# Kernel optimization log

Measured on AMD Instinct MI355X. Metric: run time of the kernel, lower is better.

## Reference

```python
import jax, jax.numpy as jnp
import numpy as np
from math import factorial, pi, sqrt

LMAX = 5
MUL_IN = 128
NUM_CHANNELS = 4
NUM_RADII = 20
RES_BETA = 180
RES_ALPHA = 359
IRREPS_DIM = (LMAX + 1) ** 2  # 36
NUM_GRAPHS = 32
NUM_SPECIES = 5


def _sh_grid_matrix():
    """Real spherical harmonics evaluated on a Gauss-Legendre (beta) x uniform (alpha) grid.

    Returns Y of shape [RES_BETA, RES_ALPHA, IRREPS_DIM]; this is the dense form of
    e3nn's to_s2grid (Legendre x Fourier) transform matrix.
    """
    y, _ = np.polynomial.legendre.leggauss(RES_BETA)  # y = cos(beta), quadrature='gausslegendre'
    alpha = 2.0 * np.pi * np.arange(RES_ALPHA) / RES_ALPHA
    # Associated Legendre P_l^m(y) (no Condon-Shortley), shape [l, m, RES_BETA]
    P = np.zeros((LMAX + 1, LMAX + 1, RES_BETA))
    P[0, 0] = 1.0
    sy = np.sqrt(np.maximum(1.0 - y * y, 0.0))
    for m in range(1, LMAX + 1):
        P[m, m] = (2 * m - 1) * sy * P[m - 1, m - 1]
    for m in range(LMAX):
        P[m + 1, m] = (2 * m + 1) * y * P[m, m]
    for m in range(LMAX + 1):
        for l in range(m + 2, LMAX + 1):
            P[l, m] = ((2 * l - 1) * y * P[l - 1, m] - (l + m - 1) * P[l - 2, m]) / (l - m)
    Y = np.zeros((RES_BETA, RES_ALPHA, IRREPS_DIM))
    idx = 0
    for l in range(LMAX + 1):
        for m in range(-l, l + 1):
            am = abs(m)
            K = sqrt((2 * l + 1) / (4.0 * pi) * factorial(l - am) / factorial(l + am))
            if m == 0:
                Y[:, :, idx] = (K * P[l, 0])[:, None]
            elif m > 0:
                Y[:, :, idx] = sqrt(2.0) * K * P[l, m][:, None] * np.cos(m * alpha)[None, :]
            else:
                Y[:, :, idx] = sqrt(2.0) * K * P[l, am][:, None] * np.sin(am * alpha)[None, :]
            idx += 1
    return Y.astype(np.float32)


def setup_inputs() -> dict:
    key = jax.random.key(0)
    k1, k2, k3, k4 = jax.random.split(key, 4)
    focus = jax.random.normal(k1, (NUM_GRAPHS, MUL_IN * IRREPS_DIM), dtype=jnp.float32)
    embed_table = jax.random.normal(k2, (NUM_SPECIES, MUL_IN * (LMAX + 1)), dtype=jnp.float32)
    linear_weights = jax.random.normal(k3, (LMAX + 1, MUL_IN, NUM_RADII * NUM_CHANNELS), dtype=jnp.float32)
    target_species = jax.random.randint(k4, (NUM_GRAPHS,), 0, NUM_SPECIES)
    return {
        "focus_node_embeddings": focus,
        "embed_table": embed_table,
        "linear_weights": linear_weights,
        "target_species": target_species,
    }


def reference(focus_node_embeddings, embed_table, linear_weights, target_species):
    G = focus_node_embeddings.shape[0]
    Y = jnp.asarray(_sh_grid_matrix())  # [B, A, 36]
    emb = embed_table[target_species]  # [G, num_irreps = 768], one scalar per irrep channel
    inv_sqrt_fan = 1.0 / np.sqrt(MUL_IN).astype(np.float32)

    coeffs = []
    off_in, off_emb = 0, 0
    for l in range(LMAX + 1):
        dim_m = 2 * l + 1
        # irreps-block view: [G, mul_in, 2l+1]
        x_l = focus_node_embeddings[:, off_in:off_in + MUL_IN * dim_m].reshape(G, MUL_IN, dim_m)
        # per-irrep scalar gating (target_species_embeddings * focus_node_embeddings)
        x_l = x_l * emb[:, off_emb:off_emb + MUL_IN, None]
        # equivariant Linear: mixes multiplicities only, per m, fan-in normalized
        y_l = jnp.einsum("gim,io->gom", x_l, linear_weights[l]) * inv_sqrt_fan
        # mul_to_axis(num_channels) then mul_to_axis(num_radii)
        coeffs.append(y_l.reshape(G, NUM_CHANNELS, NUM_RADII, dim_m))
        off_in += MUL_IN * dim_m
        off_emb += MUL_IN
    position_coeffs = jnp.concatenate(coeffs, axis=-1)  # [G, C, R, 36]

    # to_s2grid: coefficients -> spherical grid signal
    grid = jnp.einsum("gcri,bai->gcrba", position_coeffs, Y)  # [G, C, R, B, A]
    # logsumexp over channels, then max-normalize per graph
    logits = jax.scipy.special.logsumexp(grid, axis=1)  # [G, R, B, A]
    logits = logits - logits.max(axis=(-3, -2, -1), keepdims=True)
    return position_coeffs, logits
```

## Files before the change

kernel.cpp:

```cpp
#include <hip/hip_runtime.h>

#define G_N    32
#define MUL    128
#define RADII  20
#define CH     4
#define RES_B  180
#define RES_A  359
#define IDIM   36
#define COEFF_N (G_N*CH*RADII*IDIM)
#define NCHUNK 5
#define BCH_BLK 36
#define BCH_W   9

typedef float v2f __attribute__((ext_vector_type(2)));

__device__ __forceinline__ float fexp2(float x){
#if __has_builtin(__builtin_amdgcn_exp2f)
  return __builtin_amdgcn_exp2f(x);
#else
  return exp2f(x);
#endif
}
__device__ __forceinline__ float flog2(float x){
#if __has_builtin(__builtin_amdgcn_logf)
  return __builtin_amdgcn_logf(x);
#else
  return log2f(x);
#endif
}
__device__ __forceinline__ unsigned enc_f(float f){
  unsigned u = __float_as_uint(f);
  return (u & 0x80000000u) ? ~u : (u | 0x80000000u);
}
__device__ __forceinline__ float dec_f(unsigned k){
  return __uint_as_float((k & 0x80000000u) ? (k ^ 0x80000000u) : ~k);
}

__global__ __launch_bounds__(256) void fused_prep_kernel(
                              const float* __restrict__ focus, const float* __restrict__ embt,
                              const float* __restrict__ W, const int* __restrict__ tspec,
                              float* __restrict__ out,
                              float* __restrict__ PYs, float* __restrict__ Ftab){
  __shared__ double ak[RES_B + 1], bk[RES_B + 1];
  int blk = blockIdx.x;
  int t   = threadIdx.x;
  if (blk == 360){
    const double PI = 3.14159265358979323846;
    const double LOG2E = 1.4426950408889634074;
    if (t >= 2 && t <= RES_B){
      ak[t] = (2.0*t - 1.0) / (double)t;
      bk[t] = (t - 1.0) / (double)t;
    }
    __syncthreads();
    if (t < RES_B){
      int i = RES_B - 1 - t;
      double x = cos(PI * (i + 0.75) / (RES_B + 0.5));
      for (int it = 0; it < 3; ++it){
        double p0 = 1.0, p1 = x;
        for (int k = 2; k <= RES_B; ++k){
          double t1 = ak[k] * x;
          double pk = fma(t1, p1, -(bk[k] * p0));
          p0 = p1; p1 = pk;
        }
        x -= p1 * (x*x - 1.0) / ((double)RES_B * (x*p1 - p0));
      }
      double y = x;
      double sy = sqrt(fmax(1.0 - y*y, 0.0));
      double P[6][6];
      P[0][0] = 1.0;
      for (int m = 1; m < 6; ++m) P[m][m] = (2.0*m - 1.0)*sy*P[m-1][m-1];
      for (int m = 0; m < 5; ++m) P[m+1][m] = (2.0*m + 1.0)*y*P[m][m];
      for (int m = 0; m < 6; ++m)
        for (int l = m + 2; l < 6; ++l)
          P[l][m] = ((2.0*l - 1.0)*y*P[l-1][m] - (l + m - 1.0)*P[l-2][m]) / (double)(l - m);
      const double fact[11] = {1,1,2,6,24,120,720,5040,40320,362880,3628800};
      for (int l = 0; l < 6; ++l)
        for (int m = 0; m <= l; ++m){
          double K = sqrt((2.0*l + 1.0)/(4.0*PI)*fact[l-m]/fact[l+m]);
          double v = K * P[l][m] * LOG2E;
          if (m > 0) v *= sqrt(2.0);
          PYs[t*36 + l*6 + m] = (float)v;
        }
    }
    for (int a = t; a < RES_A; a += 256){
      double al = 2.0*PI*a/(double)RES_A;
      Ftab[a*12 + 0] = 1.0f;
      for (int m = 1; m <= 5; ++m){
        Ftab[a*12 + m]     = (float)cos(m*al);
        Ftab[a*12 + 5 + m] = (float)sin(m*al);
      }
      Ftab[a*12 + 11] = 0.f;
    }
  } else {
    int idx = blk * 256 + t;
    int i36 = idx % IDIM;
    int go  = idx / IDIM;
    int o   = go % (CH*RADII);
    int g   = go / (CH*RADII);
    int l   = (int)sqrtf((float)i36 + 0.5f);
    int mo  = i36 - l*l;
    int dim = 2*l + 1;
    const float* fp = focus + g*(MUL*IDIM) + MUL*l*l + mo;
    const float* ep = embt + tspec[g]*(MUL*6) + MUL*l;
    const float* wp = W + l*(MUL*80) + o;
    float s = 0.f;
    #pragma unroll 4
    for (int i = 0; i < MUL; ++i)
      s = fmaf(fp[i*dim] * ep[i], wp[i*80], s);
    out[idx] = s * 0.088388347648318447f;
  }
}

template<int WRITE>
__global__ __launch_bounds__(256, 4) void compute_kernel(const float* __restrict__ coeffs,
                          const float* __restrict__ PYs, const float* __restrict__ Ftab,
                          float* __restrict__ out, unsigned* __restrict__ gmax){
  int blk   = blockIdx.x;
  int chunk = blk % NCHUNK;
  int gr    = blk / NCHUNK;
  int r = gr % RADII;
  int g = gr / RADII;
  int tid  = threadIdx.x;
  int wave = tid >> 6, lane = tid & 63;
  int b0   = chunk * BCH_BLK;

  __shared__ float cv[CH][IDIM];
  __shared__ __align__(16) float tmpa[BCH_BLK][12][4];
  __shared__ float wred[4];

  for (int v = tid; v < CH*IDIM; v += 256){
    int c = v / IDIM, i = v % IDIM;
    cv[c][i] = coeffs[((g*CH + c)*RADII + r)*IDIM + i];
  }
  float nsub = 0.f;
  if (WRITE) nsub = -flog2(dec_f(gmax[g])) * 0.69314718055994531f;
  float f0[11], f1[11], f2[11];
  {
    const float4* Fq = reinterpret_cast<const float4*>(Ftab);
    float4 a0 = Fq[lane*3],       a1 = Fq[lane*3+1],       a2 = Fq[lane*3+2];
    float4 b0v = Fq[(lane+64)*3], b1 = Fq[(lane+64)*3+1],  b2 = Fq[(lane+64)*3+2];
    float4 c0 = Fq[(lane+128)*3], c1 = Fq[(lane+128)*3+1], c2 = Fq[(lane+128)*3+2];
    f0[0]=a0.x; f0[1]=a0.y; f0[2]=a0.z; f0[3]=a0.w; f0[4]=a1.x; f0[5]=a1.y;
    f0[6]=a1.z; f0[7]=a1.w; f0[8]=a2.x; f0[9]=a2.y; f0[10]=a2.z;
    f1[0]=b0v.x; f1[1]=b0v.y; f1[2]=b0v.z; f1[3]=b0v.w; f1[4]=b1.x; f1[5]=b1.y;
    f1[6]=b1.z; f1[7]=b1.w; f1[8]=b2.x; f1[9]=b2.y; f1[10]=b2.z;
    f2[0]=c0.x; f2[1]=c0.y; f2[2]=c0.z; f2[3]=c0.w; f2[4]=c1.x; f2[5]=c1.y;
    f2[6]=c1.z; f2[7]=c1.w; f2[8]=c2.x; f2[9]=c2.y; f2[10]=c2.z;
  }
  __syncthreads();

  for (int v = tid; v < BCH_BLK*44; v += 256){
    int bl = v / 44, cm = v % 44;
    int c = cm / 11, mm = cm % 11;
    int am, ii;
    if (mm == 0)      { am = 0;      ii = 0;        }
    else if (mm <= 5) { am = mm;     ii = mm;       }
    else              { am = mm - 5; ii = -(mm-5);  }
    const float* py = PYs + (b0 + bl)*36 + am;
    float s = 0.f;
    for (int l = am; l < 6; ++l)
      s = fmaf(cv[c][l*l + l + ii], py[l*6], s);
    tmpa[bl][mm][c] = s;
  }
  __syncthreads();

  const float LN2 = 0.69314718055994531f;
  float smx[3] = {0.f, 0.f, 0.f};
  bool tail_ok = (lane < 52);
  float* row = out + ((size_t)gr*RES_B + b0 + wave*BCH_W)*RES_A;
  for (int bl = 0; bl < BCH_W; ++bl){
    const float4* tq = reinterpret_cast<const float4*>(&tmpa[wave*BCH_W + bl][0][0]);
    v2f C01[3], C23[3], S01[3], S23[3];
    {
      float4 qv = tq[0];
      v2f a = {qv.x, qv.y}, b = {qv.z, qv.w};
      #pragma unroll
      for (int k = 0; k < 3; ++k){ C01[k] = a; C23[k] = b; }
    }
    #pragma unroll
    for (int mm = 1; mm <= 5; ++mm){
      float4 qv = tq[mm];
      v2f a = {qv.x, qv.y}, b = {qv.z, qv.w};
      C01[0] = __builtin_elementwise_fma(a, (v2f){f0[mm], f0[mm]}, C01[0]);
      C23[0] = __builtin_elementwise_fma(b, (v2f){f0[mm], f0[mm]}, C23[0]);
      C01[1] = __builtin_elementwise_fma(a, (v2f){f1[mm], f1[mm]}, C01[1]);
      C23[1] = __builtin_elementwise_fma(b, (v2f){f1[mm], f1[mm]}, C23[1]);
      C01[2] = __builtin_elementwise_fma(a, (v2f){f2[mm], f2[mm]}, C01[2]);
      C23[2] = __builtin_elementwise_fma(b, (v2f){f2[mm], f2[mm]}, C23[2]);
    }
    {
      float4 qv = tq[6];
      v2f a = {qv.x, qv.y}, b = {qv.z, qv.w};
      S01[0] = a * (v2f){f0[6], f0[6]};  S23[0] = b * (v2f){f0[6], f0[6]};
      S01[1] = a * (v2f){f1[6], f1[6]};  S23[1] = b * (v2f){f1[6], f1[6]};
      S01[2] = a * (v2f){f2[6], f2[6]};  S23[2] = b * (v2f){f2[6], f2[6]};
    }
    #pragma unroll
    for (int mm = 7; mm <= 10; ++mm){
      float4 qv = tq[mm];
      v2f a = {qv.x, qv.y}, b = {qv.z, qv.w};
      S01[0] = __builtin_elementwise_fma(a, (v2f){f0[mm], f0[mm]}, S01[0]);
      S23[0] = __builtin_elementwise_fma(b, (v2f){f0[mm], f0[mm]}, S23[0]);
      S01[1] = __builtin_elementwise_fma(a, (v2f){f1[mm], f1[mm]}, S01[1]);
      S23[1] = __builtin_elementwise_fma(b, (v2f){f1[mm], f1[mm]}, S23[1]);
      S01[2] = __builtin_elementwise_fma(a, (v2f){f2[mm], f2[mm]}, S01[2]);
      S23[2] = __builtin_elementwise_fma(b, (v2f){f2[mm], f2[mm]}, S23[2]);
    }
    #pragma unroll
    for (int k = 0; k < 3; ++k){
      v2f hp0 = C01[k] + S01[k], hp1 = C23[k] + S23[k];
      v2f hm0 = C01[k] - S01[k], hm1 = C23[k] - S23[k];
      float sp = (fexp2(hp0.x) + fexp2(hp0.y)) + (fexp2(hp1.x) + fexp2(hp1.y));
      float sm = (fexp2(hm0.x) + fexp2(hm0.y)) + (fexp2(hm1.x) + fexp2(hm1.y));
      if (WRITE){
        if (k < 2 || tail_ok){
          int p = lane + 64*k;
          row[p] = fmaf(flog2(sp), LN2, nsub);
          if (p) row[359 - p] = fmaf(flog2(sm), LN2, nsub);
        }
      } else {
        smx[k] = fmaxf(smx[k], fmaxf(sp, sm));
      }
    }
    row += RES_A;
  }
  if (!WRITE){
    float smax = fmaxf(fmaxf(smx[0], smx[1]), smx[2]);
    #pragma unroll
    for (int off = 32; off > 0; off >>= 1)
      smax = fmaxf(smax, __shfl_xor(smax, off, 64));
    if (lane == 0) wred[wave] = smax;
    __syncthreads();
    if (tid == 0){
      float m = fmaxf(fmaxf(wred[0], wred[1]), fmaxf(wred[2], wred[3]));
      atomicMax(gmax + g, enc_f(m));
    }
  }
}

extern "C" void kernel_launch(void* const* d_in, const int* in_sizes, int n_in,
                              void* d_out, int out_size, void* d_ws, size_t ws_size,
                              hipStream_t stream){
  const float* focus = (const float*)d_in[0];
  const float* embt  = (const float*)d_in[1];
  const float* W     = (const float*)d_in[2];
  const int*   tspec = (const int*)d_in[3];
  float* out = (float*)d_out;
  float* ws  = (float*)d_ws;
  unsigned* gmax = (unsigned*)d_ws;
  float* PYs  = ws + 32;
  float* Ftab = ws + 32 + RES_B*36;

  hipMemsetAsync(d_ws, 0, 128, stream);
  fused_prep_kernel<<<361, 256, 0, stream>>>(focus, embt, W, tspec, out, PYs, Ftab);
  float* logits = out + COEFF_N;
  compute_kernel<0><<<G_N*RADII*NCHUNK, 256, 0, stream>>>(out, PYs, Ftab, logits, gmax);
  compute_kernel<1><<<G_N*RADII*NCHUNK, 256, 0, stream>>>(out, PYs, Ftab, logits, gmax);
}
```

Before: 163.0 us.

## Replace two-pass recompute with single compute pass plus half-precision staging and fixup

The compute kernel previously ran twice, once to find the per-graph max and once to write normalized logits. It now runs once, recording the max and writing unnormalized log2 values either to an fp16 workspace buffer (when the workspace is large enough) or directly to the fp32 output. A streaming fixup kernel then converts to natural log and subtracts the per-graph max. This drops the recomputation of the grid transform and exp/log at the cost of an extra memory pass, and storing values in fp16 loses precision in the logits.

```diff
diff --git a/kernel.cpp b/kernel.cpp
--- a/kernel.cpp
+++ b/kernel.cpp
@@ -11,6 +11,8 @@
 #define NCHUNK 5
 #define BCH_BLK 36
 #define BCH_W   9
+#define PER_G   (RADII*RES_B*RES_A)
+#define TOT_L   (G_N*PER_G)
 
 typedef float v2f __attribute__((ext_vector_type(2)));
 
@@ -111,10 +113,11 @@
   }
 }
 
-template<int WRITE>
+template<int HALF>
 __global__ __launch_bounds__(256, 4) void compute_kernel(const float* __restrict__ coeffs,
                           const float* __restrict__ PYs, const float* __restrict__ Ftab,
-                          float* __restrict__ out, unsigned* __restrict__ gmax){
+                          _Float16* __restrict__ hbuf, float* __restrict__ fbuf,
+                          unsigned* __restrict__ gmax){
   int blk   = blockIdx.x;
   int chunk = blk % NCHUNK;
   int gr    = blk / NCHUNK;
@@ -132,8 +135,6 @@
     int c = v / IDIM, i = v % IDIM;
     cv[c][i] = coeffs[((g*CH + c)*RADII + r)*IDIM + i];
   }
-  float nsub = 0.f;
-  if (WRITE) nsub = -flog2(dec_f(gmax[g])) * 0.69314718055994531f;
   float f0[11], f1[11], f2[11];
   {
     const float4* Fq = reinterpret_cast<const float4*>(Ftab);
@@ -164,10 +165,9 @@
   }
   __syncthreads();
 
-  const float LN2 = 0.69314718055994531f;
-  float smx[3] = {0.f, 0.f, 0.f};
+  float smx[3] = {-1e30f, -1e30f, -1e30f};
   bool tail_ok = (lane < 52);
-  float* row = out + ((size_t)gr*RES_B + b0 + wave*BCH_W)*RES_A;
+  size_t rowoff = ((size_t)gr*RES_B + b0 + wave*BCH_W)*RES_A;
   for (int bl = 0; bl < BCH_W; ++bl){
     const float4* tq = reinterpret_cast<const float4*>(&tmpa[wave*BCH_W + bl][0][0]);
     v2f C01[3], C23[3], S01[3], S23[3];
@@ -212,28 +212,71 @@
       v2f hm0 = C01[k] - S01[k], hm1 = C23[k] - S23[k];
       float sp = (fexp2(hp0.x) + fexp2(hp0.y)) + (fexp2(hp1.x) + fexp2(hp1.y));
       float sm = (fexp2(hm0.x) + fexp2(hm0.y)) + (fexp2(hm1.x) + fexp2(hm1.y));
-      if (WRITE){
-        if (k < 2 || tail_ok){
-          int p = lane + 64*k;
-          row[p] = fmaf(flog2(sp), LN2, nsub);
-          if (p) row[359 - p] = fmaf(flog2(sm), LN2, nsub);
+      float hvp = flog2(sp), hvm = flog2(sm);
+      smx[k] = fmaxf(smx[k], fmaxf(hvp, hvm));
+      if (k < 2 || tail_ok){
+        int p = lane + 64*k;
+        if (HALF){
+          hbuf[rowoff + p] = (_Float16)hvp;
+          if (p) hbuf[rowoff + 359 - p] = (_Float16)hvm;
+        } else {
+          fbuf[rowoff + p] = hvp;
+          if (p) fbuf[rowoff + 359 - p] = hvm;
         }
-      } else {
-        smx[k] = fmaxf(smx[k], fmaxf(sp, sm));
       }
     }
-    row += RES_A;
-  }
-  if (!WRITE){
-    float smax = fmaxf(fmaxf(smx[0], smx[1]), smx[2]);
-    #pragma unroll
-    for (int off = 32; off > 0; off >>= 1)
-      smax = fmaxf(smax, __shfl_xor(smax, off, 64));
-    if (lane == 0) wred[wave] = smax;
-    __syncthreads();
-    if (tid == 0){
-      float m = fmaxf(fmaxf(wred[0], wred[1]), fmaxf(wred[2], wred[3]));
-      atomicMax(gmax + g, enc_f(m));
+    rowoff += RES_A;
+  }
+  float smax = fmaxf(fmaxf(smx[0], smx[1]), smx[2]);
+  #pragma unroll
+  for (int off = 32; off > 0; off >>= 1)
+    smax = fmaxf(smax, __shfl_xor(smax, off, 64));
+  if (lane == 0) wred[wave] = smax;
+  __syncthreads();
+  if (tid == 0){
+    float m = fmaxf(fmaxf(wred[0], wred[1]), fmaxf(wred[2], wred[3]));
+    atomicMax(gmax + g, enc_f(m));
+  }
+}
+
+template<int HALF>
+__global__ __launch_bounds__(256) void fixup_kernel(const _Float16* __restrict__ hbuf,
+                                                    float* __restrict__ logits,
+                                                    const unsigned* __restrict__ gmax){
+  const float LN2 = 0.69314718055994531f;
+  if (HALF){
+    const int total8 = TOT_L/8;
+    const uint4* hv = reinterpret_cast<const uint4*>(hbuf);
+    float4* l4 = reinterpret_cast<float4*>(logits);
+    int stride = gridDim.x * 256;
+    for (int i = blockIdx.x * 256 + threadIdx.x; i < total8; i += stride){
+      int g = (int)(((unsigned)i) / (PER_G/8));
+      float nsub = -dec_f(gmax[g]) * LN2;
+      union { uint4 u; _Float16 h[8]; } un;
+      un.u = hv[i];
+      float4 o0, o1;
+      o0.x = fmaf((float)un.h[0], LN2, nsub);
+      o0.y = fmaf((float)un.h[1], LN2, nsub);
+      o0.z = fmaf((float)un.h[2], LN2, nsub);
+      o0.w = fmaf((float)un.h[3], LN2, nsub);
+      o1.x = fmaf((float)un.h[4], LN2, nsub);
+      o1.y = fmaf((float)un.h[5], LN2, nsub);
+      o1.z = fmaf((float)un.h[6], LN2, nsub);
+      o1.w = fmaf((float)un.h[7], LN2, nsub);
+      l4[2*i]   = o0;
+      l4[2*i+1] = o1;
+    }
+  } else {
+    const int total4 = TOT_L/4;
+    float4* l4 = reinterpret_cast<float4*>(logits);
+    int stride = gridDim.x * 256;
+    for (int i = blockIdx.x * 256 + threadIdx.x; i < total4; i += stride){
+      int g = (int)(((unsigned)i) / (PER_G/4));
+      float nsub = -dec_f(gmax[g]) * LN2;
+      float4 v = l4[i];
+      v.x = fmaf(v.x, LN2, nsub); v.y = fmaf(v.y, LN2, nsub);
+      v.z = fmaf(v.z, LN2, nsub); v.w = fmaf(v.w, LN2, nsub);
+      l4[i] = v;
     }
   }
 }
@@ -250,10 +293,19 @@
   unsigned* gmax = (unsigned*)d_ws;
   float* PYs  = ws + 32;
   float* Ftab = ws + 32 + RES_B*36;
+  _Float16* hbuf = (_Float16*)(ws + 16384);
+
+  const size_t need = 16384*4 + (size_t)TOT_L*2;
+  const bool use_half = (ws_size >= need);
 
   hipMemsetAsync(d_ws, 0, 128, stream);
   fused_prep_kernel<<<361, 256, 0, stream>>>(focus, embt, W, tspec, out, PYs, Ftab);
   float* logits = out + COEFF_N;
-  compute_kernel<0><<<G_N*RADII*NCHUNK, 256, 0, stream>>>(out, PYs, Ftab, logits, gmax);
-  compute_kernel<1><<<G_N*RADII*NCHUNK, 256, 0, stream>>>(out, PYs, Ftab, logits, gmax);
-}
+  if (use_half){
+    compute_kernel<1><<<G_N*RADII*NCHUNK, 256, 0, stream>>>(out, PYs, Ftab, hbuf, logits, gmax);
+    fixup_kernel<1><<<2048, 256, 0, stream>>>(hbuf, logits, gmax);
+  } else {
+    compute_kernel<0><<<G_N*RADII*NCHUNK, 256, 0, stream>>>(out, PYs, Ftab, hbuf, logits, gmax);
+    fixup_kernel<0><<<2048, 256, 0, stream>>>(hbuf, logits, gmax);
+  }
+}
```

Measured after the change: 145.7 us. 10.6% less time.
